# Kernel optimization log

Hardware: AMD Instinct MI355X
Metric: run time of the kernel (lower is better)

## Reference

```python
import jax, jax.numpy as jnp
import numpy as np

B, W, N, K = 8, 16, 40, 10
DN = DL = 128
DE = 128
H = 4
NEG_SLOPE = 0.2


def _build_graph():
    # per-graph ring adjacency: i -> (i+d) % N for d=1..K, in dense_to_sparse order (src-major, dst ascending)
    src0, dst0 = [], []
    for i in range(N):
        ds = sorted(((i + d) % N) for d in range(1, K + 1))
        src0 += [i] * K
        dst0 += ds
    src0 = np.asarray(src0)
    dst0 = np.asarray(dst0)
    G = B * W
    Epg = N * K
    offs = np.arange(G)[:, None] * N
    node_adj = np.stack([(src0[None] + offs).reshape(-1), (dst0[None] + offs).reshape(-1)])
    # line graph: for each node, pair every incoming edge with every outgoing edge (torch repeat/tile order)
    a0, a1, fe = [], [], []
    for num in range(N):
        inc = np.nonzero(dst0 == num)[0]
        out = np.nonzero(src0 == num)[0]
        a0.append(np.repeat(inc, out.size))
        a1.append(np.tile(out, inc.size))
        fe.append(np.full(inc.size * out.size, num))
    a0, a1, fe = np.concatenate(a0), np.concatenate(a1), np.concatenate(fe)
    keep = a0 != a1  # remove_self_loops (no-op here, kept for fidelity)
    a0, a1, fe = a0[keep], a1[keep], fe[keep]
    eoffs = np.arange(G)[:, None] * Epg
    edge_adj = np.stack([(a0[None] + eoffs).reshape(-1), (a1[None] + eoffs).reshape(-1)])
    edge_efea = (fe[None] + offs).reshape(-1)
    return node_adj, edge_adj, edge_efea


def setup_inputs() -> dict:
    key = jax.random.key(0)
    node_adj, edge_adj, edge_efea = _build_graph()
    Epg = N * K
    D1 = DN + DL
    ks = jax.random.split(key, 16)

    def lin(k, fi, fo):
        return jax.random.normal(k, (fi, fo), jnp.float32) / np.sqrt(fi).astype(np.float32)

    return dict(
        x_node=jax.random.normal(ks[0], (B, W, N, DN), jnp.float32),
        x_trace=jax.random.normal(ks[1], (B, W, Epg, DE), jnp.float32),
        x_log=jax.random.normal(ks[2], (B, W, N, DL), jnp.float32),
        node_adj=jnp.asarray(node_adj, jnp.int32),
        edge_adj=jnp.asarray(edge_adj, jnp.int32),
        edge_efea=jnp.asarray(edge_efea, jnp.int32),
        Wl1=lin(ks[3], D1, D1), bl1=jnp.zeros((D1,), jnp.float32),
        Wr1=lin(ks[4], D1, D1), br1=jnp.zeros((D1,), jnp.float32),
        We1=lin(ks[5], DE, D1), be1=jnp.zeros((D1,), jnp.float32),
        att1=jax.random.normal(ks[6], (H, D1 // H), jnp.float32) / np.sqrt(D1 // H).astype(np.float32),
        bias1=jnp.zeros((D1,), jnp.float32),
        Wl2=lin(ks[7], DE, DE), bl2=jnp.zeros((DE,), jnp.float32),
        Wr2=lin(ks[8], DE, DE), br2=jnp.zeros((DE,), jnp.float32),
        We2=lin(ks[9], D1, DE), be2=jnp.zeros((DE,), jnp.float32),
        att2=jax.random.normal(ks[10], (H, DE // H), jnp.float32) / np.sqrt(DE // H).astype(np.float32),
        bias2=jnp.zeros((DE,), jnp.float32),
    )


def _gatv2(x, edge_index, edge_attr, Wl, bl, Wr, br, We, be, att, bias, heads):
    """PyG GATv2Conv (eval mode, add_self_loops=False, concat heads)."""
    n = x.shape[0]
    HC = Wl.shape[1]
    C = HC // heads
    xl = (x @ Wl + bl).reshape(n, heads, C)  # source transform
    xr = (x @ Wr + br).reshape(n, heads, C)  # target transform
    src, dst = edge_index[0], edge_index[1]
    ea = (edge_attr @ We + be).reshape(-1, heads, C)
    m = jax.nn.leaky_relu(xl[src] + xr[dst] + ea, NEG_SLOPE)  # [E,H,C]
    logits = jnp.einsum('ehc,hc->eh', m, att)
    # segment softmax over incoming edges per target node
    mx = jax.ops.segment_max(logits, dst, num_segments=n)
    mx = jnp.where(jnp.isfinite(mx), mx, 0.0)
    ex = jnp.exp(logits - mx[dst])
    den = jax.ops.segment_sum(ex, dst, num_segments=n)
    alpha = ex / (den[dst] + 1e-16)
    out = jax.ops.segment_sum(alpha[:, :, None] * xl[src], dst, num_segments=n)  # [n,H,C]
    return out.reshape(n, HC) + bias


def reference(x_node, x_trace, x_log, node_adj, edge_adj, edge_efea,
              Wl1, bl1, Wr1, br1, We1, be1, att1, bias1,
              Wl2, bl2, Wr2, br2, We2, be2, att2, bias2):
    b, w, n, dn = x_node.shape
    dl = x_log.shape[-1]
    node = jnp.concatenate([x_node, x_log], axis=-1).reshape(-1, dn + dl)  # [G*N, Dn+Dl]
    trace = x_trace.reshape(-1, x_trace.shape[-1])                          # [G*Epg, De]
    node = _gatv2(node, node_adj, trace, Wl1, bl1, Wr1, br1, We1, be1, att1, bias1, H)
    trace = _gatv2(trace, edge_adj, node[edge_efea], Wl2, bl2, Wr2, br2, We2, be2, att2, bias2, H)
    x_node_o = node[:, :dn].reshape(b, w, n, dn)
    x_trace_o = trace.reshape(b, w, -1, trace.shape[-1])
    x_log_o = node[:, dn:].reshape(b, w, n, dl)
    return (x_node_o, x_trace_o, x_log_o)
```

## Files before the change

kernel.cpp:

```cpp
#include <hip/hip_runtime.h>
#include <hip/hip_bf16.h>

#define D1 256
#define DE 128
#define KDEG 10
#define NPG 40
#define EPG 400
#define LOG2E 1.44269504088896340736f

typedef __attribute__((ext_vector_type(8))) short short8;
typedef __attribute__((ext_vector_type(4))) float f32x4;

static inline int cdiv(size_t a, int b) { return (int)((a + b - 1) / b); }
static inline size_t al256(size_t x) { return (x + 255) & ~(size_t)255; }

__device__ __forceinline__ short f2b(float x) {
  __hip_bfloat16 h = __float2bfloat16(x);
  return *reinterpret_cast<short*>(&h);
}

__device__ __forceinline__ short8 cvt8(const float* __restrict__ src) {
  float4 v0 = *(const float4*)src;
  float4 v1 = *(const float4*)(src + 4);
  short8 t;
  t[0] = f2b(v0.x); t[1] = f2b(v0.y); t[2] = f2b(v0.z); t[3] = f2b(v0.w);
  t[4] = f2b(v1.x); t[5] = f2b(v1.y); t[6] = f2b(v1.z); t[7] = f2b(v1.w);
  return t;
}

__global__ __launch_bounds__(256) void k_setup(const float* __restrict__ xn,
                                               const float* __restrict__ xlg,
                                               const float* __restrict__ xtr,
                                               const float* __restrict__ Wl1,
                                               const float* __restrict__ Wr1,
                                               const float* __restrict__ We1,
                                               const float* __restrict__ Wl2,
                                               const float* __restrict__ Wr2,
                                               const float* __restrict__ We2,
                                               const float* __restrict__ bl1,
                                               const float* __restrict__ br1,
                                               const float* __restrict__ be1,
                                               const float* __restrict__ bl2,
                                               const float* __restrict__ br2,
                                               int* __restrict__ cnt,
                                               short* __restrict__ Xb,
                                               short* __restrict__ xtr_b,
                                               short* __restrict__ WT12,
                                               short* __restrict__ WTall,
                                               short* __restrict__ We2T,
                                               float* __restrict__ blr1,
                                               float* __restrict__ bfull,
                                               int NN, int NE) {
  size_t idx = (size_t)blockIdx.x * 256 + threadIdx.x;
  size_t n;
  n = (size_t)NN;           if (idx < n) { cnt[idx] = 0; return; }              idx -= n;
  n = (size_t)NN * 32;
  if (idx < n) {
    int row = (int)(idx >> 5), q = (int)(idx & 31);
    const float* src = (q < 16) ? &xn[(size_t)row * 128 + q * 8]
                                : &xlg[(size_t)row * 128 + (q - 16) * 8];
    *(short8*)&Xb[(size_t)row * 256 + q * 8] = cvt8(src);
    return;
  }
  idx -= n;
  n = (size_t)NE * 16;
  if (idx < n) {
    *(short8*)&xtr_b[idx * 8] = cvt8(&xtr[idx * 8]);
    return;
  }
  idx -= n;
  n = 512 * 256;
  if (idx < n) {
    int nn = (int)(idx >> 8), k = (int)(idx & 255);
    float v = (nn < 256) ? Wl1[(size_t)k * 256 + nn] : Wr1[(size_t)k * 256 + (nn - 256)];
    WT12[idx] = f2b(v);
    return;
  }
  idx -= n;
  n = 512 * 128;
  if (idx < n) {
    int nn = (int)(idx >> 7), k = (int)(idx & 127);
    float v;
    if (nn < 256)      v = We1[(size_t)k * 256 + nn];
    else if (nn < 384) v = Wl2[(size_t)k * 128 + (nn - 256)];
    else               v = Wr2[(size_t)k * 128 + (nn - 384)];
    WTall[idx] = f2b(v);
    return;
  }
  idx -= n;
  n = 128 * 256;
  if (idx < n) {
    int nn = (int)(idx >> 8), k = (int)(idx & 255);
    We2T[idx] = f2b(We2[(size_t)k * 128 + nn]);
    return;
  }
  idx -= n;
  n = 512;
  if (idx < n) { blr1[idx] = (idx < 256) ? bl1[idx] : br1[idx - 256]; return; }
  idx -= n;
  n = 512;
  if (idx < n) {
    bfull[idx] = (idx < 256) ? be1[idx] : (idx < 384 ? bl2[idx - 256] : br2[idx - 384]);
  }
}

__global__ __launch_bounds__(256) void k_build_inc(const int* __restrict__ adj,
                                                   int* __restrict__ cnt,
                                                   int* __restrict__ inc, int NE) {
  int e = blockIdx.x * 256 + threadIdx.x;
  if (e >= NE) return;
  int dst = adj[NE + e];
  int slot = atomicAdd(&cnt[dst], 1);
  inc[dst * KDEG + slot] = e;
}

__global__ __launch_bounds__(256) void k_gemm_mfma64(const short* __restrict__ A,
                                                     const short* __restrict__ WT,
                                                     const float* __restrict__ bias,
                                                     float* __restrict__ C,
                                                     int M, int K, int N) {
  __shared__ __align__(16) short As[64][40];
  __shared__ __align__(16) short Bs[64][40];
  const int tid = threadIdx.x;
  const int wave = tid >> 6, lane = tid & 63;
  const int quad = lane >> 4, l16 = lane & 15;
  const int m0 = blockIdx.y * 64, n0 = blockIdx.x * 64;
  const int wm = (wave & 1) * 32, wn = (wave >> 1) * 32;
  f32x4 acc[2][2] = {};
  for (int k0 = 0; k0 < K; k0 += 32) {
    {
      int r = tid >> 2, kc = (tid & 3) << 3;
      *(short8*)&As[r][kc] = *(const short8*)&A[(size_t)(m0 + r) * K + (k0 + kc)];
      *(short8*)&Bs[r][kc] = *(const short8*)&WT[(size_t)(n0 + r) * K + (k0 + kc)];
    }
    __syncthreads();
    short8 af[2], bf[2];
    #pragma unroll
    for (int mt = 0; mt < 2; ++mt)
      af[mt] = *(const short8*)&As[wm + mt * 16 + l16][quad << 3];
    #pragma unroll
    for (int nt = 0; nt < 2; ++nt)
      bf[nt] = *(const short8*)&Bs[wn + nt * 16 + l16][quad << 3];
    #pragma unroll
    for (int mt = 0; mt < 2; ++mt)
      #pragma unroll
      for (int nt = 0; nt < 2; ++nt)
        acc[mt][nt] = __builtin_amdgcn_mfma_f32_16x16x32_bf16(
            af[mt], bf[nt], acc[mt][nt], 0, 0, 0);
    __syncthreads();
  }
  #pragma unroll
  for (int nt = 0; nt < 2; ++nt) {
    int col = n0 + wn + nt * 16 + l16;
    float bs = bias[col];
    #pragma unroll
    for (int mt = 0; mt < 2; ++mt) {
      int row = m0 + wm + mt * 16 + (quad << 2);
      #pragma unroll
      for (int r = 0; r < 4; ++r)
        C[(size_t)(row + r) * N + col] = acc[mt][nt][r] + bs;
    }
  }
}

__global__ __launch_bounds__(256) void k_gemm_mega(const short* __restrict__ A,
                                                   const short* __restrict__ WT,
                                                   const float* __restrict__ bfull,
                                                   const float* __restrict__ att1,
                                                   const int* __restrict__ adj,
                                                   const float* __restrict__ xlr1,
                                                   float* __restrict__ logit1,
                                                   float* __restrict__ pool2,
                                                   int NE) {
  const int K = 128;
  struct SmemGemm { short As[128][40]; short Bs[128][40]; };
  struct SmemEpi  { int sdst[128]; float sxl[14][132]; float sxr[NPG][132]; };
  __shared__ __align__(16) union { SmemGemm g; SmemEpi e; } sm;
  const int tid = threadIdx.x;
  const int wave = tid >> 6, lane = tid & 63;
  const int quad = lane >> 4, l16 = lane & 15;
  int bid = blockIdx.x;
  int l = (bid & 7) * ((int)gridDim.x >> 3) + (bid >> 3);
  const int n0 = (l & 3) << 7;
  const int m0 = (l >> 2) << 7;
  const int wm = (wave & 1) * 64, wn = (wave >> 1) * 64;
  f32x4 acc[4][4] = {};
  for (int k0 = 0; k0 < K; k0 += 32) {
    #pragma unroll
    for (int s = 0; s < 2; ++s) {
      int ch = tid + s * 256;
      int r = ch >> 2, kc = (ch & 3) << 3;
      *(short8*)&sm.g.As[r][kc] = *(const short8*)&A[(size_t)(m0 + r) * K + (k0 + kc)];
      *(short8*)&sm.g.Bs[r][kc] = *(const short8*)&WT[(size_t)(n0 + r) * K + (k0 + kc)];
    }
    __syncthreads();
    short8 af[4], bf[4];
    #pragma unroll
    for (int mt = 0; mt < 4; ++mt)
      af[mt] = *(const short8*)&sm.g.As[wm + mt * 16 + l16][quad << 3];
    #pragma unroll
    for (int nt = 0; nt < 4; ++nt)
      bf[nt] = *(const short8*)&sm.g.Bs[wn + nt * 16 + l16][quad << 3];
    #pragma unroll
    for (int mt = 0; mt < 4; ++mt)
      #pragma unroll
      for (int nt = 0; nt < 4; ++nt)
        acc[mt][nt] = __builtin_amdgcn_mfma_f32_16x16x32_bf16(
            af[mt], bf[nt], acc[mt][nt], 0, 0, 0);
    __syncthreads();
  }
  if (n0 < 256) {
    const int gl = m0 / EPG;
    const int gh = (m0 + 127) / EPG;
    const int slo = m0 / KDEG;
    const int nrl = (m0 + 127) / KDEG - slo + 1;
    if (tid < 128) sm.e.sdst[tid] = adj[NE + m0 + tid];
    for (int s = tid; s < nrl * 128; s += 256) {
      int row = s >> 7, c = s & 127;
      sm.e.sxl[row][c] = xlr1[(size_t)(slo + row) * 512 + n0 + c];
    }
    const int h = (n0 + wn) >> 6;
    float attv[4], bev[4];
    int ccl[4];
    #pragma unroll
    for (int nt = 0; nt < 4; ++nt) {
      int col = n0 + wn + nt * 16 + l16;
      ccl[nt] = col - n0;
      attv[nt] = att1[col] * LOG2E;
      bev[nt] = bfull[col];
    }
    for (int g = gl; g <= gh; ++g) {
      __syncthreads();
      for (int s = tid; s < NPG * 128; s += 256) {
        int row = s >> 7, c = s & 127;
        sm.e.sxr[row][c] = xlr1[(size_t)(g * NPG + row) * 512 + 256 + n0 + c];
      }
      __syncthreads();
      const int elo = g * EPG, ehi = elo + EPG;
      #pragma unroll
      for (int mt = 0; mt < 4; ++mt) {
        #pragma unroll
        for (int r = 0; r < 4; ++r) {
          int le = wm + mt * 16 + (quad << 2) + r;
          int e = m0 + le;
          if (e < elo || e >= ehi) continue;
          int srow = e / KDEG - slo;
          int d = sm.e.sdst[le];
          int drow = d - g * NPG;
          float p = 0.f;
          #pragma unroll
          for (int nt = 0; nt < 4; ++nt) {
            float v = acc[mt][nt][r] + bev[nt] + sm.e.sxl[srow][ccl[nt]]
                    + sm.e.sxr[drow][ccl[nt]];
            v = (v > 0.f) ? v : 0.2f * v;
            p += v * attv[nt];
          }
          p += __shfl_xor(p, 1, 64);
          p += __shfl_xor(p, 2, 64);
          p += __shfl_xor(p, 4, 64);
          p += __shfl_xor(p, 8, 64);
          if (l16 == 0) {
            logit1[(size_t)e * 4 + h] = exp2f(p);
          }
        }
      }
    }
  } else {
    #pragma unroll
    for (int nt = 0; nt < 4; ++nt) {
      int col = n0 + wn + nt * 16 + l16;
      float bs = bfull[col];
      int pcol = col - 256;
      #pragma unroll
      for (int mt = 0; mt < 4; ++mt) {
        int row = m0 + wm + mt * 16 + (quad << 2);
        #pragma unroll
        for (int r = 0; r < 4; ++r)
          pool2[(size_t)(row + r) * 256 + pcol] = acc[mt][nt][r] + bs;
      }
    }
  }
}

__global__ __launch_bounds__(256) void k_agg1(const int* __restrict__ adj,
                                              const int* __restrict__ inc,
                                              const float* __restrict__ xlr1,
                                              const float* __restrict__ logit1,
                                              const float* __restrict__ bias1,
                                              short* __restrict__ nodeoutb,
                                              float* __restrict__ out_node,
                                              float* __restrict__ out_log) {
  int u = blockIdx.x, c = threadIdx.x;
  __shared__ int se[KDEG], ssrc[KDEG];
  __shared__ float slg[KDEG * 4];
  if (c < KDEG) se[c] = inc[u * KDEG + c];
  __syncthreads();
  if (c < KDEG) ssrc[c] = adj[se[c]];
  else if (c >= 64 && c < 64 + KDEG * 4) {
    int t = c - 64;
    slg[t] = logit1[(size_t)se[t >> 2] * 4 + (t & 3)];
  }
  __syncthreads();
  int h = c >> 6;
  float den = 0.f;
  #pragma unroll
  for (int j = 0; j < KDEG; ++j) den += slg[j * 4 + h];
  float rden = 1.f / (den + 1e-16f);
  float acc = 0.f;
  #pragma unroll
  for (int j = 0; j < KDEG; ++j)
    acc += slg[j * 4 + h] * xlr1[(size_t)ssrc[j] * 512 + c];
  float val = acc * rden + bias1[c];
  nodeoutb[(size_t)u * D1 + c] = f2b(val);
  if (c < 128) out_node[(size_t)u * 128 + c] = val;
  else         out_log[(size_t)u * 128 + (c - 128)] = val;
}

__global__ __launch_bounds__(256) void k_gat2_v4(const int* __restrict__ eadj,
                                                 const int* __restrict__ efea,
                                                 const float* __restrict__ pool2,
                                                 const float* __restrict__ nproj,
                                                 const float* __restrict__ att2,
                                                 const float* __restrict__ bias2,
                                                 float* __restrict__ out_trace,
                                                 int NL) {
  int gi = blockIdx.x;
  size_t le0 = (size_t)gi * 100;
  int t = threadIdx.x;
  const int wave = t >> 6, lane = t & 63;
  __shared__ int ein[KDEG], eout[KDEG], nvs;
  __shared__ float xs[KDEG][132];
  __shared__ float rs[KDEG][132];
  __shared__ float as_[DE];
  __shared__ float exs[400];
  __shared__ float rdn[40];
  if (t < KDEG)          ein[t] = eadj[le0 + (size_t)t * KDEG];
  else if (t < 2 * KDEG) eout[t - KDEG] = eadj[(size_t)NL + le0 + (t - KDEG)];
  else if (t == 255)     nvs = efea[le0];
  __syncthreads();
  int nv = nvs;
  for (int s = t; s < 320; s += 256) {
    int j = s >> 5, q = (s & 31) << 2;
    *(float4*)&xs[j][q] = *(const float4*)&pool2[(size_t)ein[j] * 256 + q];
    float4 tr4 = *(const float4*)&pool2[(size_t)eout[j] * 256 + 128 + q];
    float4 ea4 = *(const float4*)&nproj[(size_t)nv * DE + q];
    float4 r;
    r.x = tr4.x + ea4.x; r.y = tr4.y + ea4.y;
    r.z = tr4.z + ea4.z; r.w = tr4.w + ea4.w;
    *(float4*)&rs[j][q] = r;
  }
  if (t < 32) {
    float4 a4 = *(const float4*)&att2[t << 2];
    float4 o;
    o.x = a4.x * LOG2E; o.y = a4.y * LOG2E;
    o.z = a4.z * LOG2E; o.w = a4.w * LOG2E;
    *(float4*)&as_[t << 2] = o;
  }
  __syncthreads();
  {
    int h = wave;
    const float* aa = &as_[h << 5];
    for (int idx = lane; idx < 100; idx += 64) {
      int j = idx / 10;
      int o = idx - j * 10;
      const float* xa = &xs[j][h << 5];
      const float* ra = &rs[o][h << 5];
      float p = 0.f;
      #pragma unroll
      for (int i = 0; i < 32; i += 4) {
        float4 xv = *(const float4*)&xa[i];
        float4 rv = *(const float4*)&ra[i];
        float4 av = *(const float4*)&aa[i];
        float v;
        v = xv.x + rv.x; v = (v > 0.f) ? v : 0.2f * v; p += v * av.x;
        v = xv.y + rv.y; v = (v > 0.f) ? v : 0.2f * v; p += v * av.y;
        v = xv.z + rv.z; v = (v > 0.f) ? v : 0.2f * v; p += v * av.z;
        v = xv.w + rv.w; v = (v > 0.f) ? v : 0.2f * v; p += v * av.w;
      }
      exs[(j * 10 + o) * 4 + h] = exp2f(p);
    }
  }
  __syncthreads();
  if (t < 40) {
    float d = 0.f;
    #pragma unroll
    for (int j = 0; j < KDEG; ++j) d += exs[(j * 10 + (t >> 2)) * 4 + (t & 3)];
    rdn[t] = 1.f / d;
  }
  __syncthreads();
  {
    int c = t & 127, h = c >> 5, oh = (t >> 7) * 5;
    float bsv = bias2[c];
    #pragma unroll
    for (int oo = 0; oo < 5; ++oo) {
      int o = oh + oo;
      float acc = 0.f;
      #pragma unroll
      for (int j = 0; j < KDEG; ++j)
        acc += exs[(j * 10 + o) * 4 + h] * xs[j][c];
      out_trace[(size_t)eout[o] * DE + c] = acc * rdn[o * 4 + h] + bsv;
    }
  }
}

extern "C" void kernel_launch(void* const* d_in, const int* in_sizes, int n_in,
                              void* d_out, int out_size, void* d_ws, size_t ws_size,
                              hipStream_t stream) {
  const float* x_node   = (const float*)d_in[0];
  const float* x_trace  = (const float*)d_in[1];
  const float* x_log    = (const float*)d_in[2];
  const int*   node_adj = (const int*)d_in[3];
  const int*   edge_adj = (const int*)d_in[4];
  const int*   edge_efea= (const int*)d_in[5];
  const float* Wl1 = (const float*)d_in[6];
  const float* bl1 = (const float*)d_in[7];
  const float* Wr1 = (const float*)d_in[8];
  const float* br1 = (const float*)d_in[9];
  const float* We1 = (const float*)d_in[10];
  const float* be1 = (const float*)d_in[11];
  const float* att1 = (const float*)d_in[12];
  const float* bias1 = (const float*)d_in[13];
  const float* Wl2 = (const float*)d_in[14];
  const float* bl2 = (const float*)d_in[15];
  const float* Wr2 = (const float*)d_in[16];
  const float* br2 = (const float*)d_in[17];
  const float* We2 = (const float*)d_in[18];
  const float* be2 = (const float*)d_in[19];
  const float* att2 = (const float*)d_in[20];
  const float* bias2 = (const float*)d_in[21];

  const int NN = in_sizes[0] / 128;
  const int NE = in_sizes[1] / 128;
  const int NL = in_sizes[5];

  char* p = (char*)d_ws;
  float* pool2   = (float*)p; p += al256((size_t)NE * 256 * 4);
  float* xlr1    = (float*)p; p += al256((size_t)NN * 512 * 4);
  short* Xb      = (short*)p; p += al256((size_t)NN * D1 * 2);
  short* xtr_b   = (short*)p; p += al256((size_t)NE * DE * 2);
  short* nodeoutb= (short*)p; p += al256((size_t)NN * D1 * 2);
  float* nproj   = (float*)p; p += al256((size_t)NN * DE * 4);
  float* logit1  = (float*)p; p += al256((size_t)NE * 4 * 4);
  int*   inc     = (int*)p;   p += al256((size_t)NN * KDEG * 4);
  int*   cnt     = (int*)p;   p += al256((size_t)NN * 4);
  short* WT12    = (short*)p; p += al256((size_t)512 * 256 * 2);
  short* WTall   = (short*)p; p += al256((size_t)512 * 128 * 2);
  short* We2T    = (short*)p; p += al256((size_t)128 * 256 * 2);
  float* blr1    = (float*)p; p += al256(512 * 4);
  float* bfull   = (float*)p; p += al256(512 * 4);
  (void)ws_size;

  float* out_node  = (float*)d_out;
  float* out_trace = out_node + (size_t)NN * 128;
  float* out_log   = out_trace + (size_t)NE * 128;

  {
    size_t total = (size_t)NN + (size_t)NN * 32 + (size_t)NE * 16 +
                   512 * 256 + 512 * 128 + 128 * 256 + 512 + 512;
    k_setup<<<cdiv(total, 256), 256, 0, stream>>>(x_node, x_log, x_trace,
                                                  Wl1, Wr1, We1, Wl2, Wr2, We2,
                                                  bl1, br1, be1, bl2, br2,
                                                  cnt, Xb, xtr_b,
                                                  WT12, WTall, We2T, blr1, bfull,
                                                  NN, NE);
  }
  k_build_inc<<<cdiv(NE, 256), 256, 0, stream>>>(node_adj, cnt, inc, NE);

  k_gemm_mfma64<<<dim3(512 / 64, NN / 64), 256, 0, stream>>>(Xb, WT12, blr1, xlr1,
                                                             NN, D1, 512);

  k_gemm_mega<<<4 * (NE / 128), 256, 0, stream>>>(xtr_b, WTall, bfull, att1,
                                                  node_adj, xlr1, logit1,
                                                  pool2, NE);

  k_agg1<<<NN, 256, 0, stream>>>(node_adj, inc, xlr1, logit1, bias1,
                                 nodeoutb, out_node, out_log);

  k_gemm_mfma64<<<dim3(DE / 64, NN / 64), 256, 0, stream>>>(nodeoutb, We2T, be2,
                                                            nproj, NN, D1, DE);
  k_gat2_v4<<<NN, 256, 0, stream>>>(edge_adj, edge_efea, pool2, nproj,
                                    att2, bias2, out_trace, NL);
}
```

Measured before the change: 231.6 us.

## Split mega GEMM into logit kernel and separate pool2 GEMM; register-prefetch tiles

The combined trace GEMM kernel, which produced both the layer-1 attention logits and the layer-2 pool projection, is split. A logit-only kernel covers the first 256 output columns, and the pool2 projection becomes a separate 64x64 MFMA GEMM launched after the node-projection GEMM. Both GEMM kernels now prefetch the next K-slice into registers while the current slice is computed, hiding global load latency behind the MFMAs. The split removes the divergent n0 branch and shrinks the grid of the critical-path logit kernel. In exchange it adds a kernel launch and uses the smaller tile for the pool2 GEMM, which means less operand reuse.

```diff
diff --git a/kernel.cpp b/kernel.cpp
--- a/kernel.cpp
+++ b/kernel.cpp
@@ -126,14 +126,18 @@
   const int quad = lane >> 4, l16 = lane & 15;
   const int m0 = blockIdx.y * 64, n0 = blockIdx.x * 64;
   const int wm = (wave & 1) * 32, wn = (wave >> 1) * 32;
+  const int r = tid >> 2, kc = (tid & 3) << 3;
   f32x4 acc[2][2] = {};
+  short8 pa = *(const short8*)&A[(size_t)(m0 + r) * K + kc];
+  short8 pb = *(const short8*)&WT[(size_t)(n0 + r) * K + kc];
   for (int k0 = 0; k0 < K; k0 += 32) {
-    {
-      int r = tid >> 2, kc = (tid & 3) << 3;
-      *(short8*)&As[r][kc] = *(const short8*)&A[(size_t)(m0 + r) * K + (k0 + kc)];
-      *(short8*)&Bs[r][kc] = *(const short8*)&WT[(size_t)(n0 + r) * K + (k0 + kc)];
-    }
-    __syncthreads();
+    *(short8*)&As[r][kc] = pa;
+    *(short8*)&Bs[r][kc] = pb;
+    __syncthreads();
+    if (k0 + 32 < K) {
+      pa = *(const short8*)&A[(size_t)(m0 + r) * K + (k0 + 32 + kc)];
+      pb = *(const short8*)&WT[(size_t)(n0 + r) * K + (k0 + 32 + kc)];
+    }
     short8 af[2], bf[2];
     #pragma unroll
     for (int mt = 0; mt < 2; ++mt)
@@ -157,21 +161,20 @@
     for (int mt = 0; mt < 2; ++mt) {
       int row = m0 + wm + mt * 16 + (quad << 2);
       #pragma unroll
-      for (int r = 0; r < 4; ++r)
-        C[(size_t)(row + r) * N + col] = acc[mt][nt][r] + bs;
-    }
-  }
-}
-
-__global__ __launch_bounds__(256) void k_gemm_mega(const short* __restrict__ A,
-                                                   const short* __restrict__ WT,
-                                                   const float* __restrict__ bfull,
-                                                   const float* __restrict__ att1,
-                                                   const int* __restrict__ adj,
-                                                   const float* __restrict__ xlr1,
-                                                   float* __restrict__ logit1,
-                                                   float* __restrict__ pool2,
-                                                   int NE) {
+      for (int rr = 0; rr < 4; ++rr)
+        C[(size_t)(row + rr) * N + col] = acc[mt][nt][rr] + bs;
+    }
+  }
+}
+
+__global__ __launch_bounds__(256) void k_logit(const short* __restrict__ A,
+                                               const short* __restrict__ WT,
+                                               const float* __restrict__ bfull,
+                                               const float* __restrict__ att1,
+                                               const int* __restrict__ adj,
+                                               const float* __restrict__ xlr1,
+                                               float* __restrict__ logit1,
+                                               int NE) {
   const int K = 128;
   struct SmemGemm { short As[128][40]; short Bs[128][40]; };
   struct SmemEpi  { int sdst[128]; float sxl[14][132]; float sxr[NPG][132]; };
@@ -181,19 +184,28 @@
   const int quad = lane >> 4, l16 = lane & 15;
   int bid = blockIdx.x;
   int l = (bid & 7) * ((int)gridDim.x >> 3) + (bid >> 3);
-  const int n0 = (l & 3) << 7;
-  const int m0 = (l >> 2) << 7;
+  const int n0 = (l & 1) << 7;
+  const int m0 = (l >> 1) << 7;
   const int wm = (wave & 1) * 64, wn = (wave >> 1) * 64;
+  const int rr0 = tid >> 2, rr1 = (tid + 256) >> 2;
+  const int kc = (tid & 3) << 3;
   f32x4 acc[4][4] = {};
+  short8 pa0 = *(const short8*)&A[(size_t)(m0 + rr0) * K + kc];
+  short8 pb0 = *(const short8*)&WT[(size_t)(n0 + rr0) * K + kc];
+  short8 pa1 = *(const short8*)&A[(size_t)(m0 + rr1) * K + kc];
+  short8 pb1 = *(const short8*)&WT[(size_t)(n0 + rr1) * K + kc];
   for (int k0 = 0; k0 < K; k0 += 32) {
-    #pragma unroll
-    for (int s = 0; s < 2; ++s) {
-      int ch = tid + s * 256;
-      int r = ch >> 2, kc = (ch & 3) << 3;
-      *(short8*)&sm.g.As[r][kc] = *(const short8*)&A[(size_t)(m0 + r) * K + (k0 + kc)];
-      *(short8*)&sm.g.Bs[r][kc] = *(const short8*)&WT[(size_t)(n0 + r) * K + (k0 + kc)];
-    }
-    __syncthreads();
+    *(short8*)&sm.g.As[rr0][kc] = pa0;
+    *(short8*)&sm.g.Bs[rr0][kc] = pb0;
+    *(short8*)&sm.g.As[rr1][kc] = pa1;
+    *(short8*)&sm.g.Bs[rr1][kc] = pb1;
+    __syncthreads();
+    if (k0 + 32 < K) {
+      pa0 = *(const short8*)&A[(size_t)(m0 + rr0) * K + (k0 + 32 + kc)];
+      pb0 = *(const short8*)&WT[(size_t)(n0 + rr0) * K + (k0 + 32 + kc)];
+      pa1 = *(const short8*)&A[(size_t)(m0 + rr1) * K + (k0 + 32 + kc)];
+      pb1 = *(const short8*)&WT[(size_t)(n0 + rr1) * K + (k0 + 32 + kc)];
+    }
     short8 af[4], bf[4];
     #pragma unroll
     for (int mt = 0; mt < 4; ++mt)
@@ -209,74 +221,58 @@
             af[mt], bf[nt], acc[mt][nt], 0, 0, 0);
     __syncthreads();
   }
-  if (n0 < 256) {
-    const int gl = m0 / EPG;
-    const int gh = (m0 + 127) / EPG;
-    const int slo = m0 / KDEG;
-    const int nrl = (m0 + 127) / KDEG - slo + 1;
-    if (tid < 128) sm.e.sdst[tid] = adj[NE + m0 + tid];
-    for (int s = tid; s < nrl * 128; s += 256) {
+  const int gl = m0 / EPG;
+  const int gh = (m0 + 127) / EPG;
+  const int slo = m0 / KDEG;
+  const int nrl = (m0 + 127) / KDEG - slo + 1;
+  if (tid < 128) sm.e.sdst[tid] = adj[NE + m0 + tid];
+  for (int s = tid; s < nrl * 128; s += 256) {
+    int row = s >> 7, c = s & 127;
+    sm.e.sxl[row][c] = xlr1[(size_t)(slo + row) * 512 + n0 + c];
+  }
+  const int h = (n0 + wn) >> 6;
+  float attv[4], bev[4];
+  int ccl[4];
+  #pragma unroll
+  for (int nt = 0; nt < 4; ++nt) {
+    int col = n0 + wn + nt * 16 + l16;
+    ccl[nt] = col - n0;
+    attv[nt] = att1[col] * LOG2E;
+    bev[nt] = bfull[col];
+  }
+  for (int g = gl; g <= gh; ++g) {
+    __syncthreads();
+    for (int s = tid; s < NPG * 128; s += 256) {
       int row = s >> 7, c = s & 127;
-      sm.e.sxl[row][c] = xlr1[(size_t)(slo + row) * 512 + n0 + c];
-    }
-    const int h = (n0 + wn) >> 6;
-    float attv[4], bev[4];
-    int ccl[4];
-    #pragma unroll
-    for (int nt = 0; nt < 4; ++nt) {
-      int col = n0 + wn + nt * 16 + l16;
-      ccl[nt] = col - n0;
-      attv[nt] = att1[col] * LOG2E;
-      bev[nt] = bfull[col];
-    }
-    for (int g = gl; g <= gh; ++g) {
-      __syncthreads();
-      for (int s = tid; s < NPG * 128; s += 256) {
-        int row = s >> 7, c = s & 127;
-        sm.e.sxr[row][c] = xlr1[(size_t)(g * NPG + row) * 512 + 256 + n0 + c];
-      }
-      __syncthreads();
-      const int elo = g * EPG, ehi = elo + EPG;
-      #pragma unroll
-      for (int mt = 0; mt < 4; ++mt) {
+      sm.e.sxr[row][c] = xlr1[(size_t)(g * NPG + row) * 512 + 256 + n0 + c];
+    }
+    __syncthreads();
+    const int elo = g * EPG, ehi = elo + EPG;
+    #pragma unroll
+    for (int mt = 0; mt < 4; ++mt) {
+      #pragma unroll
+      for (int r = 0; r < 4; ++r) {
+        int le = wm + mt * 16 + (quad << 2) + r;
+        int e = m0 + le;
+        if (e < elo || e >= ehi) continue;
+        int srow = e / KDEG - slo;
+        int d = sm.e.sdst[le];
+        int drow = d - g * NPG;
+        float p = 0.f;
         #pragma unroll
-        for (int r = 0; r < 4; ++r) {
-          int le = wm + mt * 16 + (quad << 2) + r;
-          int e = m0 + le;
-          if (e < elo || e >= ehi) continue;
-          int srow = e / KDEG - slo;
-          int d = sm.e.sdst[le];
-          int drow = d - g * NPG;
-          float p = 0.f;
-          #pragma unroll
-          for (int nt = 0; nt < 4; ++nt) {
-            float v = acc[mt][nt][r] + bev[nt] + sm.e.sxl[srow][ccl[nt]]
-                    + sm.e.sxr[drow][ccl[nt]];
-            v = (v > 0.f) ? v : 0.2f * v;
-            p += v * attv[nt];
-          }
-          p += __shfl_xor(p, 1, 64);
-          p += __shfl_xor(p, 2, 64);
-          p += __shfl_xor(p, 4, 64);
-          p += __shfl_xor(p, 8, 64);
-          if (l16 == 0) {
-            logit1[(size_t)e * 4 + h] = exp2f(p);
-          }
+        for (int nt = 0; nt < 4; ++nt) {
+          float v = acc[mt][nt][r] + bev[nt] + sm.e.sxl[srow][ccl[nt]]
+                  + sm.e.sxr[drow][ccl[nt]];
+          v = (v > 0.f) ? v : 0.2f * v;
+          p += v * attv[nt];
         }
-      }
-    }
-  } else {
-    #pragma unroll
-    for (int nt = 0; nt < 4; ++nt) {
-      int col = n0 + wn + nt * 16 + l16;
-      float bs = bfull[col];
-      int pcol = col - 256;
-      #pragma unroll
-      for (int mt = 0; mt < 4; ++mt) {
-        int row = m0 + wm + mt * 16 + (quad << 2);
-        #pragma unroll
-        for (int r = 0; r < 4; ++r)
-          pool2[(size_t)(row + r) * 256 + pcol] = acc[mt][nt][r] + bs;
+        p += __shfl_xor(p, 1, 64);
+        p += __shfl_xor(p, 2, 64);
+        p += __shfl_xor(p, 4, 64);
+        p += __shfl_xor(p, 8, 64);
+        if (l16 == 0) {
+          logit1[(size_t)e * 4 + h] = exp2f(p);
+        }
       }
     }
   }
@@ -469,15 +465,18 @@
   k_gemm_mfma64<<<dim3(512 / 64, NN / 64), 256, 0, stream>>>(Xb, WT12, blr1, xlr1,
                                                              NN, D1, 512);
 
-  k_gemm_mega<<<4 * (NE / 128), 256, 0, stream>>>(xtr_b, WTall, bfull, att1,
-                                                  node_adj, xlr1, logit1,
-                                                  pool2, NE);
+  k_logit<<<2 * (NE / 128), 256, 0, stream>>>(xtr_b, WTall, bfull, att1,
+                                              node_adj, xlr1, logit1, NE);
 
   k_agg1<<<NN, 256, 0, stream>>>(node_adj, inc, xlr1, logit1, bias1,
                                  nodeoutb, out_node, out_log);
 
   k_gemm_mfma64<<<dim3(DE / 64, NN / 64), 256, 0, stream>>>(nodeoutb, We2T, be2,
                                                             nproj, NN, D1, DE);
+
+  k_gemm_mfma64<<<dim3(256 / 64, NE / 64), 256, 0, stream>>>(
+      xtr_b, WTall + (size_t)256 * 128, bfull + 256, pool2, NE, DE, 256);
+
   k_gat2_v4<<<NN, 256, 0, stream>>>(edge_adj, edge_efea, pool2, nproj,
                                     att2, bias2, out_trace, NL);
 }
```

New measurement: 223.4 us. 1.04x faster.
